# Performance work log

Hardware: AMD Instinct MI355X
Metric: run time of the kernel (lower is better)

Reference implementation:

```python
import jax, jax.numpy as jnp
import numpy as np

TEMPERATURE = 0.07
BASE_TEMPERATURE = 0.07
EPS = 1e-10


def setup_inputs() -> dict:
    key = jax.random.key(0)
    k1, k2, k3 = jax.random.split(key, 3)
    bsz, n_views, d = 4096, 2, 256
    features = jax.random.normal(k1, (bsz, n_views, d), dtype=jnp.float32)
    # L2-normalize views as is standard for SupCon inputs (keeps logits sane)
    features = features / jnp.linalg.norm(features, axis=-1, keepdims=True)
    va_labels = jax.random.normal(k2, (bsz, 2), dtype=jnp.float32)
    batch_belong_diaID = jax.random.randint(k3, (bsz,), 0, 512, dtype=jnp.int64)
    return {
        "features": features,
        "va_labels": va_labels,
        "batch_belong_diaID": batch_belong_diaID,
        "thres_dict": 1,
    }


def reference(features, va_labels, batch_belong_diaID, thres_dict):
    bsz, n_views, d = features.shape
    dtype = features.dtype

    # --- vectorized mask construction (replaces O(bsz^2) python loops) ---
    eye = jnp.eye(bsz, dtype=bool)
    same_dia = batch_belong_diaID[:, None] == batch_belong_diaID[None, :]
    diff = va_labels[:, None, :] - va_labels[None, :, :]          # [bsz, bsz, 2]
    euclid = jnp.sqrt(jnp.sum(diff * diff, axis=-1))              # [bsz, bsz]
    close_va = euclid < thres_dict
    # final mask: diagonal | same dialogue | VA-close (off-diag terms; diag already 1)
    mask = (eye | same_dia | close_va).astype(dtype)
    mask = jax.lax.stop_gradient(mask)  # mask build is non-differentiable in torch too

    # --- contrastive loss (contrast_mode='one') ---
    # torch.cat(torch.unbind(features, 1), 0): view-major stacking
    contrast_feature = features.transpose(1, 0, 2).reshape(n_views * bsz, d)
    anchor_feature = features[:, 0]                               # anchor_count = 1

    logits = jnp.matmul(anchor_feature, contrast_feature.T) / TEMPERATURE  # [bsz, n_views*bsz]
    logits = logits - jax.lax.stop_gradient(jnp.max(logits, axis=1, keepdims=True))

    mask_t = jnp.tile(mask, (1, n_views))                          # [bsz, n_views*bsz]
    # logits_mask: zero out self-contrast (column i for anchor row i)
    idx = jnp.arange(bsz)
    logits_mask = jnp.ones((bsz, n_views * bsz), dtype=dtype).at[idx, idx].set(0.0)
    mask_t = mask_t * logits_mask

    exp_logits = jnp.exp(logits) * logits_mask
    log_prob = logits - jnp.log(jnp.sum(exp_logits, axis=1, keepdims=True) + EPS)

    mean_log_prob_pos = jnp.sum(mask_t * log_prob, axis=1) / (jnp.sum(mask_t, axis=1) + EPS)
    loss = jnp.mean(-mean_log_prob_pos)  # anchor_count=1 -> plain mean over bsz
    return loss
```

## Files before the change

### kernel.cpp

```cpp
#include <hip/hip_runtime.h>
#include <hip/hip_bf16.h>

#define BSZ   4096
#define NCON  8192
#define DFEAT 256
#define C2    20.60992914f
#define LN2   0.6931471806f

#define BJM 16
#define BI 64
#define NJT 16
#define JSTRIP_M (NJT * BJM)

typedef __attribute__((ext_vector_type(8))) short short8;
typedef __attribute__((ext_vector_type(4))) float f32x4;

__device__ __forceinline__ unsigned short f2bf(float f) {
    __hip_bfloat16 h = __float2bfloat16(f);
    return *reinterpret_cast<unsigned short*>(&h);
}

__device__ __forceinline__ void gload_lds16(const void* g, void* l) {
    __builtin_amdgcn_global_load_lds(
        (const __attribute__((address_space(1))) unsigned int*)g,
        (__attribute__((address_space(3))) unsigned int*)l,
        16, 0, 0);
}

__device__ __forceinline__ void gload_reg16(const void* p, short8& dst) {
    unsigned long long a = (unsigned long long)p;
    asm volatile("global_load_dwordx4 %0, %1, off"
                 : "=v"(dst) : "v"(a));
}


__global__ __launch_bounds__(256) void k_prep(const float* __restrict__ feat,
                                              unsigned short* __restrict__ con,
                                              float* __restrict__ acc) {
    int idx = blockIdx.x * 256 + threadIdx.x;
    int e = idx * 4;
    int j = e >> 8;
    int k = e & 255;
    int src = (j < BSZ) ? ((j * 2) * DFEAT + k)
                        : (((j - BSZ) * 2 + 1) * DFEAT + k);
    float4 f = *(const float4*)(feat + src);
    ushort4 o;
    o.x = f2bf(f.x); o.y = f2bf(f.y); o.z = f2bf(f.z); o.w = f2bf(f.w);
    *(ushort4*)(con + e) = o;
    if (idx < 3 * BSZ) acc[idx] = 0.0f;
}

__global__ __launch_bounds__(256) void k_main(const __hip_bfloat16* __restrict__ conp,
                                              const float* __restrict__ va,
                                              const int* __restrict__ dia,
                                              const int* __restrict__ thr_ptr,
                                              float* __restrict__ Srow,
                                              float* __restrict__ Arow,
                                              float* __restrict__ Brow) {
    __shared__ short lX[2][2][BJM * DFEAT];
    __shared__ float s_vjx[JSTRIP_M], s_vjy[JSTRIP_M];
    __shared__ int   s_dj[JSTRIP_M];

    const int tid  = threadIdx.x;
    const int lane = tid & 63;
    const int wv   = tid >> 6;
    const int l15  = lane & 15;
    const int hi   = lane >> 4;
    const int jmbase = blockIdx.x * JSTRIP_M;
    const int ibase  = blockIdx.y * BI + wv * 16;
    const short* cs = (const short*)conp;

    auto stageX = [&](int buf, int jt) {
        #pragma unroll
        for (int v = 0; v < 2; ++v) {
            #pragma unroll
            for (int q = 0; q < 2; ++q) {
                int e   = q * 2048 + tid * 8;
                int col = e & 63;
                int row = (e >> 6) & 15;
                int k2  = e >> 10;
                int scol = col ^ ((row & 7) << 3);
                gload_lds16(cs + (size_t)(jmbase + jt * BJM + row + v * BSZ) * DFEAT
                               + k2 * 64 + scol,
                            &lX[buf][v][e]);
            }
        }
    };

    stageX(0, 0);

    const short* yrow0 = cs + (size_t)(ibase + l15) * DFEAT + hi * 8;
    short8 y[8];
    #pragma unroll
    for (int s = 0; s < 8; ++s)
        gload_reg16(yrow0 + s * 32, y[s]);

    if (tid < JSTRIP_M) {
        int jm = jmbase + tid;
        s_vjx[tid] = va[2 * jm]; s_vjy[tid] = va[2 * jm + 1]; s_dj[tid] = dia[jm];
    }

    int raw = *thr_ptr;
    float t_ = (raw > 0 && raw < 100000) ? (float)raw : __int_as_float(raw);
    float thres2 = t_ * t_;

    const int i_g = ibase + l15;
    float vix = va[2 * i_g], viy = va[2 * i_g + 1];
    int   di  = dia[i_g];

    float sp = 0.f, ap = 0.f, bp = 0.f;

    __syncthreads();
    asm volatile("s_waitcnt vmcnt(0)" ::: "memory");
    __builtin_amdgcn_sched_barrier(0);

    for (int jt = 0; jt < NJT; ++jt) {
        const int cur = jt & 1;
        if (jt < NJT - 1) stageX(cur ^ 1, jt + 1);

        f32x4 acc0 = (f32x4){0.f, 0.f, 0.f, 0.f};
        f32x4 acc1 = (f32x4){0.f, 0.f, 0.f, 0.f};

        #pragma unroll
        for (int s = 0; s < 8; ++s) {
            const int base = (s >> 1) * 2048;
            const int colb = (s & 1) * 64 + hi * 16;
            const int row  = l15;
            const int off  = base + row * 128 + (colb ^ ((row & 7) << 4));
            short8 x0 = *(const short8*)((const char*)&lX[cur][0][0] + off);
            short8 x1 = *(const short8*)((const char*)&lX[cur][1][0] + off);
            acc0 = __builtin_amdgcn_mfma_f32_16x16x32_bf16(x0, y[s], acc0, 0, 0, 0);
            acc1 = __builtin_amdgcn_mfma_f32_16x16x32_bf16(x1, y[s], acc1, 0, 0, 0);
        }

        const int jt0 = jt * BJM;
        #pragma unroll
        for (int r = 0; r < 4; ++r) {
            const int jl  = jt0 + hi * 4 + r;
            const int jmg = jmbase + jl;
            float vjx = s_vjx[jl], vjy = s_vjy[jl];
            int dj = s_dj[jl];
            float l0 = __builtin_fmaf(acc0[r], C2, -C2);
            float l1 = __builtin_fmaf(acc1[r], C2, -C2);
            float dx = vix - vjx, dy = viy - vjy;
            bool diag = (i_g == jmg);
            bool mk = diag | (di == dj) | (dx * dx + dy * dy < thres2);
            float e0 = diag ? 0.0f : exp2f(l0);
            float e1 = exp2f(l1);
            sp += e0 + e1;
            float m0 = (mk & !diag) ? 1.0f : 0.0f;
            float m1 = mk ? 1.0f : 0.0f;
            ap = __builtin_fmaf(m0, l0, ap);
            ap = __builtin_fmaf(m1, l1, ap);
            bp += m0 + m1;
        }
        __syncthreads();
    }

    sp += __shfl_xor(sp, 16, 64);  ap += __shfl_xor(ap, 16, 64);  bp += __shfl_xor(bp, 16, 64);
    sp += __shfl_xor(sp, 32, 64);  ap += __shfl_xor(ap, 32, 64);  bp += __shfl_xor(bp, 32, 64);
    if (hi == 0) {
        atomicAdd(&Srow[i_g], sp);
        atomicAdd(&Arow[i_g], ap * LN2);
        atomicAdd(&Brow[i_g], bp);
    }
}

__global__ __launch_bounds__(256) void k_final(const float* __restrict__ S,
                                               const float* __restrict__ A,
                                               const float* __restrict__ B,
                                               float* __restrict__ out) {
    __shared__ float red[256];
    float sum = 0.f;
    for (int i = threadIdx.x; i < BSZ; i += 256) {
        float b = B[i];
        float v = (A[i] - b * logf(S[i] + 1e-10f)) / (b + 1e-10f);
        sum += -v;
    }
    red[threadIdx.x] = sum;
    __syncthreads();
    for (int s = 128; s > 0; s >>= 1) {
        if (threadIdx.x < s) red[threadIdx.x] += red[threadIdx.x + s];
        __syncthreads();
    }
    if (threadIdx.x == 0) out[0] = red[0] / (float)BSZ;
}

extern "C" void kernel_launch(void* const* d_in, const int* in_sizes, int n_in,
                              void* d_out, int out_size, void* d_ws, size_t ws_size,
                              hipStream_t stream) {
    const float* feat = (const float*)d_in[0];
    const float* va   = (const float*)d_in[1];
    const int*   dia  = (const int*)d_in[2];
    const int*   thr  = (const int*)d_in[3];

    unsigned short* con = (unsigned short*)d_ws;
    float* acc = (float*)((char*)d_ws + (size_t)NCON * DFEAT * 2);
    float* out = (float*)d_out;

    k_prep<<<(NCON * DFEAT / 4 + 255) / 256, 256, 0, stream>>>(feat, con, acc);

    dim3 grid(BSZ / JSTRIP_M, BSZ / BI);
    k_main<<<grid, 256, 0, stream>>>((const __hip_bfloat16*)con, va, dia, thr,
                                     acc, acc + BSZ, acc + 2 * BSZ);

    k_final<<<1, 256, 0, stream>>>(acc, acc + BSZ, acc + 2 * BSZ, out);
}
```

Measured before the change: 49.53 us.

## Double per-wave anchor rows to reuse LDS contrast tiles across two MFMA groups

Each wave now processes 32 anchor rows (two 16-row groups) instead of 16, so every contrast tile loaded from LDS feeds four MFMAs instead of two. The block covers 128 anchor rows over a 128-column strip, which halves the grid width and keeps the grid size the same. The mask bookkeeping is simplified: one mask value covers both views, the diagonal is removed from the count in k_final via 2B-1, and MFMA issue priority is raised around the inner loop. The cost is higher register pressure from the doubled y fragments and accumulators, which may lower occupancy.

Result: slower. 51.06 us (+3.1%).

```diff
diff --git a/kernel.cpp b/kernel.cpp
--- a/kernel.cpp
+++ b/kernel.cpp
@@ -8,8 +8,8 @@
 #define LN2   0.6931471806f
 
 #define BJM 16
-#define BI 64
-#define NJT 16
+#define BI 128
+#define NJT 8
 #define JSTRIP_M (NJT * BJM)
 
 typedef __attribute__((ext_vector_type(8))) short short8;
@@ -67,7 +67,7 @@
     const int l15  = lane & 15;
     const int hi   = lane >> 4;
     const int jmbase = blockIdx.x * JSTRIP_M;
-    const int ibase  = blockIdx.y * BI + wv * 16;
+    const int ibase  = blockIdx.y * BI + wv * 32;
     const short* cs = (const short*)conp;
 
     auto stageX = [&](int buf, int jt) {
@@ -90,10 +90,12 @@
     stageX(0, 0);
 
     const short* yrow0 = cs + (size_t)(ibase + l15) * DFEAT + hi * 8;
-    short8 y[8];
+    short8 y[2][8];
     #pragma unroll
-    for (int s = 0; s < 8; ++s)
-        gload_reg16(yrow0 + s * 32, y[s]);
+    for (int n = 0; n < 2; ++n)
+        #pragma unroll
+        for (int s = 0; s < 8; ++s)
+            gload_reg16(yrow0 + (size_t)n * 16 * DFEAT + s * 32, y[n][s]);
 
     if (tid < JSTRIP_M) {
         int jm = jmbase + tid;
@@ -104,11 +106,16 @@
     float t_ = (raw > 0 && raw < 100000) ? (float)raw : __int_as_float(raw);
     float thres2 = t_ * t_;
 
-    const int i_g = ibase + l15;
-    float vix = va[2 * i_g], viy = va[2 * i_g + 1];
-    int   di  = dia[i_g];
-
-    float sp = 0.f, ap = 0.f, bp = 0.f;
+    float vix[2], viy[2]; int di[2], ig[2];
+    #pragma unroll
+    for (int n = 0; n < 2; ++n) {
+        ig[n] = ibase + n * 16 + l15;
+        vix[n] = va[2 * ig[n]]; viy[n] = va[2 * ig[n] + 1]; di[n] = dia[ig[n]];
+    }
+
+    float sp[2] = {0.f, 0.f};
+    float ap[2] = {0.f, 0.f};
+    float bp[2] = {0.f, 0.f};
 
     __syncthreads();
     asm volatile("s_waitcnt vmcnt(0)" ::: "memory");
@@ -118,9 +125,14 @@
         const int cur = jt & 1;
         if (jt < NJT - 1) stageX(cur ^ 1, jt + 1);
 
-        f32x4 acc0 = (f32x4){0.f, 0.f, 0.f, 0.f};
-        f32x4 acc1 = (f32x4){0.f, 0.f, 0.f, 0.f};
-
+        f32x4 acc[2][2];
+        #pragma unroll
+        for (int v = 0; v < 2; ++v)
+            #pragma unroll
+            for (int n = 0; n < 2; ++n)
+                acc[v][n] = (f32x4){0.f, 0.f, 0.f, 0.f};
+
+        __builtin_amdgcn_s_setprio(1);
         #pragma unroll
         for (int s = 0; s < 8; ++s) {
             const int base = (s >> 1) * 2048;
@@ -129,9 +141,13 @@
             const int off  = base + row * 128 + (colb ^ ((row & 7) << 4));
             short8 x0 = *(const short8*)((const char*)&lX[cur][0][0] + off);
             short8 x1 = *(const short8*)((const char*)&lX[cur][1][0] + off);
-            acc0 = __builtin_amdgcn_mfma_f32_16x16x32_bf16(x0, y[s], acc0, 0, 0, 0);
-            acc1 = __builtin_amdgcn_mfma_f32_16x16x32_bf16(x1, y[s], acc1, 0, 0, 0);
-        }
+            #pragma unroll
+            for (int n = 0; n < 2; ++n) {
+                acc[0][n] = __builtin_amdgcn_mfma_f32_16x16x32_bf16(x0, y[n][s], acc[0][n], 0, 0, 0);
+                acc[1][n] = __builtin_amdgcn_mfma_f32_16x16x32_bf16(x1, y[n][s], acc[1][n], 0, 0, 0);
+            }
+        }
+        __builtin_amdgcn_s_setprio(0);
 
         const int jt0 = jt * BJM;
         #pragma unroll
@@ -140,29 +156,34 @@
             const int jmg = jmbase + jl;
             float vjx = s_vjx[jl], vjy = s_vjy[jl];
             int dj = s_dj[jl];
-            float l0 = __builtin_fmaf(acc0[r], C2, -C2);
-            float l1 = __builtin_fmaf(acc1[r], C2, -C2);
-            float dx = vix - vjx, dy = viy - vjy;
-            bool diag = (i_g == jmg);
-            bool mk = diag | (di == dj) | (dx * dx + dy * dy < thres2);
-            float e0 = diag ? 0.0f : exp2f(l0);
-            float e1 = exp2f(l1);
-            sp += e0 + e1;
-            float m0 = (mk & !diag) ? 1.0f : 0.0f;
-            float m1 = mk ? 1.0f : 0.0f;
-            ap = __builtin_fmaf(m0, l0, ap);
-            ap = __builtin_fmaf(m1, l1, ap);
-            bp += m0 + m1;
+            #pragma unroll
+            for (int n = 0; n < 2; ++n) {
+                float l0 = __builtin_fmaf(acc[0][n][r], C2, -C2);
+                float l1 = __builtin_fmaf(acc[1][n][r], C2, -C2);
+                float dx = vix[n] - vjx, dy = viy[n] - vjy;
+                bool diag = (ig[n] == jmg);
+                bool mk = (di[n] == dj) | (dx * dx + dy * dy < thres2);
+                float e0 = diag ? 0.0f : exp2f(l0);
+                float e1 = exp2f(l1);
+                sp[n] += e0 + e1;
+                float mm = mk ? 1.0f : 0.0f;
+                ap[n] = __builtin_fmaf(mm, l0 + l1, ap[n]);
+                bp[n] += mm;
+            }
         }
         __syncthreads();
     }
 
-    sp += __shfl_xor(sp, 16, 64);  ap += __shfl_xor(ap, 16, 64);  bp += __shfl_xor(bp, 16, 64);
-    sp += __shfl_xor(sp, 32, 64);  ap += __shfl_xor(ap, 32, 64);  bp += __shfl_xor(bp, 32, 64);
-    if (hi == 0) {
-        atomicAdd(&Srow[i_g], sp);
-        atomicAdd(&Arow[i_g], ap * LN2);
-        atomicAdd(&Brow[i_g], bp);
+    #pragma unroll
+    for (int n = 0; n < 2; ++n) {
+        float s = sp[n], a = ap[n], b = bp[n];
+        s += __shfl_xor(s, 16, 64);  a += __shfl_xor(a, 16, 64);  b += __shfl_xor(b, 16, 64);
+        s += __shfl_xor(s, 32, 64);  a += __shfl_xor(a, 32, 64);  b += __shfl_xor(b, 32, 64);
+        if (hi == 0) {
+            atomicAdd(&Srow[ig[n]], s);
+            atomicAdd(&Arow[ig[n]], a * LN2);
+            atomicAdd(&Brow[ig[n]], b);
+        }
     }
 }
 
@@ -173,7 +194,7 @@
     __shared__ float red[256];
     float sum = 0.f;
     for (int i = threadIdx.x; i < BSZ; i += 256) {
-        float b = B[i];
+        float b = 2.0f * B[i] - 1.0f;
         float v = (A[i] - b * logf(S[i] + 1e-10f)) / (b + 1e-10f);
         sum += -v;
     }
```
